# Performance work log

Measured on AMD Instinct MI355X. Metric: run time of the kernel, lower is better.

The kernel has to match this reference:

```python
import jax, jax.numpy as jnp
import numpy as np

D = 128  # head dim

def setup_inputs() -> dict:
    key = jax.random.key(0)
    k1, k2, k3, k4, k5 = jax.random.split(key, 5)
    B, N, M, C1, C2 = 4, 4096, 4096, 1024, 1024
    x = jax.random.normal(k1, (B, N, C1), dtype=jnp.float32)
    y = jax.random.normal(k2, (B, M, C2), dtype=jnp.float32)
    # Linear(c, d, bias=False): out = inp @ W where W is [c, d]
    Wq = jax.random.normal(k3, (C1, D), dtype=jnp.float32) / np.sqrt(C1)
    Wk = jax.random.normal(k4, (C2, D), dtype=jnp.float32) / np.sqrt(C2)
    Wv = jax.random.normal(k5, (C2, D), dtype=jnp.float32) / np.sqrt(C2)
    return {"x": x, "y": y, "Wq": Wq, "Wk": Wk, "Wv": Wv}

def reference(x, y, Wq, Wk, Wv):
    q = x @ Wq                               # [B, N, d]
    k = y @ Wk                               # [B, M, d]
    v = y @ Wv                               # [B, M, d]
    scale = 1.0 / jnp.sqrt(jnp.asarray(D, dtype=q.dtype))
    a = jnp.einsum('bnd,bmd->bnm', q, k) * scale
    a = jax.nn.softmax(a, axis=-1)           # softmax FIRST
    a = jnp.triu(a, k=1)                     # post-softmax causal mask (keeps strict upper)
    out = jnp.einsum('bnm,bmd->bnd', a, v)   # [B, N, d]
    return out
```

## Files before the change

### kernel.cpp

```cpp
#include <hip/hip_runtime.h>
#include <hip/hip_bf16.h>
#include <stdint.h>


typedef __attribute__((ext_vector_type(8))) __bf16    bf16x8;
typedef __attribute__((ext_vector_type(4))) float     floatx4;
typedef __attribute__((ext_vector_type(8))) uint16_t  u16x8;
typedef __attribute__((ext_vector_type(4))) uint32_t  u32x4;

#define DEVFN __device__ __forceinline__

DEVFN uint16_t f32_to_bf16(float f) {
  uint32_t u = __builtin_bit_cast(uint32_t, f);
  u += 0x7FFFu + ((u >> 16) & 1u);
  return (uint16_t)(u >> 16);
}

DEVFN uint32_t bcast(float f) { return __builtin_bit_cast(uint32_t, f); }

DEVFN uint32_t pack2_bf16(float a, float b) {
  return ((bcast(a) + 0x8000u) >> 16) | ((bcast(b) + 0x8000u) & 0xFFFF0000u);
}

DEVFN u32x4 pack_bf16_8(float4 a0, float4 a1) {
  u32x4 o;
  o[0] = pack2_bf16(a0.x, a0.y);
  o[1] = pack2_bf16(a0.z, a0.w);
  o[2] = pack2_bf16(a1.x, a1.y);
  o[3] = pack2_bf16(a1.z, a1.w);
  return o;
}

DEVFN void gl2lds16(const void* g, void* l) {
  __builtin_amdgcn_global_load_lds(
      (const __attribute__((address_space(1))) void*)g,
      (__attribute__((address_space(3))) void*)l, 16, 0, 0);
}

__global__ __launch_bounds__(256) void wt_kernel(
    const float* __restrict__ Wq, const float* __restrict__ Wk,
    const float* __restrict__ Wv, uint16_t* __restrict__ wt) {
  int tid = blockIdx.x * 256 + threadIdx.x;
  int mat = tid >> 14;
  int rem = tid & 16383;
  int n  = rem & 127;
  int k0 = rem >> 7;
  const float* W = (mat == 0) ? Wq : ((mat == 1) ? Wk : Wv);
  u16x8 v;
#pragma unroll
  for (int j = 0; j < 8; ++j) v[j] = f32_to_bf16(W[(k0 * 8 + j) * 128 + n]);
  *(u16x8*)&wt[mat * (128 * 1024) + n * 1024 + k0 * 8] = v;
}

__global__ __launch_bounds__(256) void qkv_kernel(
    const float* __restrict__ x, const float* __restrict__ y,
    const uint16_t* __restrict__ wt, uint16_t* __restrict__ q,
    uint16_t* __restrict__ k, uint16_t* __restrict__ vt) {
  constexpr int LDT = 72;
  constexpr int ABUF = 128 * LDT;
  __shared__ __align__(16) uint16_t sA[2 * ABUF];
  __shared__ __align__(16) uint16_t sW[2 * ABUF];
  const int t = threadIdx.x;
  const int mat = blockIdx.y, rt = blockIdx.x;
  const float* A = (mat == 0) ? x : y;
  const uint16_t* Wt = wt + mat * (128 * 1024);
  const int lane = t & 63, wv = t >> 6;
  const int cidx = lane & 15, quad = lane >> 4;
  const int sr = t >> 3;
  const int sc = (t & 7) * 8;
  const int Arow0 = rt * 128;

  floatx4 acc[2][8];
#pragma unroll
  for (int rg = 0; rg < 2; ++rg)
#pragma unroll
    for (int ng = 0; ng < 8; ++ng) acc[rg][ng] = (floatx4){0.f, 0.f, 0.f, 0.f};

  float4 a0r[4], a1r[4];
  u16x8 wr[4];
#pragma unroll
  for (int u = 0; u < 4; ++u) {
    int row = u * 32 + sr;
    const float* ap = &A[(size_t)(Arow0 + row) * 1024 + sc];
    a0r[u] = *(const float4*)ap;
    a1r[u] = *(const float4*)(ap + 4);
    wr[u]  = *(const u16x8*)&Wt[row * 1024 + sc];
  }
#pragma unroll
  for (int u = 0; u < 4; ++u) {
    int row = u * 32 + sr;
    *(u32x4*)&sA[row * LDT + sc] = pack_bf16_8(a0r[u], a1r[u]);
    *(u16x8*)&sW[row * LDT + sc] = wr[u];
  }
  __syncthreads();

  for (int kt = 0; kt < 16; ++kt) {
    const int cur = kt & 1, nxt = cur ^ 1;
    if (kt < 15) {
      const int kc = (kt + 1) * 64;
#pragma unroll
      for (int u = 0; u < 4; ++u) {
        int row = u * 32 + sr;
        const float* ap = &A[(size_t)(Arow0 + row) * 1024 + kc + sc];
        a0r[u] = *(const float4*)ap;
        a1r[u] = *(const float4*)(ap + 4);
        wr[u]  = *(const u16x8*)&Wt[row * 1024 + kc + sc];
      }
    }
    bf16x8 af[2][2];
#pragma unroll
    for (int rg = 0; rg < 2; ++rg)
#pragma unroll
      for (int ks = 0; ks < 2; ++ks)
        af[rg][ks] = *(const bf16x8*)
            &sA[cur * ABUF + (wv * 32 + rg * 16 + cidx) * LDT + ks * 32 + quad * 8];
#pragma unroll
    for (int ng = 0; ng < 8; ++ng) {
      bf16x8 b0 = *(const bf16x8*)&sW[cur * ABUF + (ng * 16 + cidx) * LDT + quad * 8];
      bf16x8 b1 = *(const bf16x8*)&sW[cur * ABUF + (ng * 16 + cidx) * LDT + 32 + quad * 8];
#pragma unroll
      for (int rg = 0; rg < 2; ++rg) {
        acc[rg][ng] = __builtin_amdgcn_mfma_f32_16x16x32_bf16(af[rg][0], b0, acc[rg][ng], 0, 0, 0);
        acc[rg][ng] = __builtin_amdgcn_mfma_f32_16x16x32_bf16(af[rg][1], b1, acc[rg][ng], 0, 0, 0);
      }
    }
    if (kt < 15) {
#pragma unroll
      for (int u = 0; u < 4; ++u) {
        int row = u * 32 + sr;
        *(u32x4*)&sA[nxt * ABUF + row * LDT + sc] = pack_bf16_8(a0r[u], a1r[u]);
        *(u16x8*)&sW[nxt * ABUF + row * LDT + sc] = wr[u];
      }
    }
    __syncthreads();
  }

  if (mat < 2) {
    uint16_t* outp = (mat == 0) ? q : k;
#pragma unroll
    for (int rg = 0; rg < 2; ++rg)
#pragma unroll
      for (int r = 0; r < 4; ++r) {
        int row = Arow0 + wv * 32 + rg * 16 + quad * 4 + r;
#pragma unroll
        for (int ng = 0; ng < 8; ++ng)
          outp[row * 128 + ng * 16 + cidx] = f32_to_bf16(acc[rg][ng][r]);
      }
  } else {
    int bq = rt >> 5;
    int mbase = (rt & 31) * 128;
#pragma unroll
    for (int rg = 0; rg < 2; ++rg)
#pragma unroll
      for (int r = 0; r < 4; ++r) {
        int m = mbase + wv * 32 + rg * 16 + quad * 4 + r;
#pragma unroll
        for (int ng = 0; ng < 8; ++ng)
          vt[(size_t)(bq * 128 + ng * 16 + cidx) * 4096 + m] = f32_to_bf16(acc[rg][ng][r]);
      }
  }
}

__global__ __launch_bounds__(256, 2) void attn_kernel(
    const uint16_t* __restrict__ q, const uint16_t* __restrict__ k,
    const uint16_t* __restrict__ vt, float* __restrict__ opart,
    float* __restrict__ lpart, int mlen, int iters) {
  constexpr int KB = 16384, VB = 16384;
  __shared__ __align__(16) uint8_t sK[2 * KB];
  __shared__ __align__(16) uint8_t sV[2 * VB];
  const int t = threadIdx.x;
  const int lane = t & 63, wv = t >> 6;
  const int cidx = lane & 15, quad = lane >> 4;
  const int qt = blockIdx.x, h = blockIdx.y, b = blockIdx.z;
  const int qmin = qt * 64 + wv * 16;
  const int mbase = h * mlen;

  const uint16_t* qb = q + (size_t)(b * 4096) * 128;
  const uint8_t* kb = (const uint8_t*)(k + (size_t)(b * 4096) * 128);
  const uint8_t* vb = (const uint8_t*)(vt + (size_t)(b * 128) * 4096);

  const float SC = 0.12751744610657223f;

  int kOffL[4], vOffL[4], kLds[4], vLds[4];
#pragma unroll
  for (int u = 0; u < 4; ++u) {
    int r  = wv * 16 + u * 4 + (lane >> 4);
    int g  = (lane & 15) ^ (r & 15);
    kOffL[u] = r * 256 + g * 16;
    kLds[u]  = (wv * 16 + u * 4) * 256;
    int rv = wv * 32 + u * 8 + (lane >> 3);
    int gv = (lane & 7) ^ (rv & 7);
    vOffL[u] = rv * 8192 + gv * 16;
    vLds[u]  = (wv * 32 + u * 8) * 128;
  }

  bf16x8 qf[4];
#pragma unroll
  for (int ks = 0; ks < 4; ++ks)
    qf[ks] = *(const bf16x8*)&qb[(qmin + cidx) * 128 + ks * 32 + quad * 8];

  floatx4 O[8];
#pragma unroll
  for (int dg = 0; dg < 8; ++dg) O[dg] = (floatx4){0.f, 0.f, 0.f, 0.f};
  float lsum = 0.f;

#pragma unroll
  for (int u = 0; u < 4; ++u) {
    gl2lds16(kb + (size_t)mbase * 256 + kOffL[u], sK + kLds[u]);
    gl2lds16(vb + (size_t)mbase * 2 + vOffL[u], sV + vLds[u]);
  }
  __syncthreads();

  for (int it = 0; it < iters; ++it) {
    const int m0 = mbase + it * 64;
    const int cur = it & 1, nxt = cur ^ 1;
    if (it + 1 < iters) {
      const int m1 = m0 + 64;
#pragma unroll
      for (int u = 0; u < 4; ++u) {
        gl2lds16(kb + (size_t)m1 * 256 + kOffL[u], sK + nxt * KB + kLds[u]);
        gl2lds16(vb + (size_t)m1 * 2 + vOffL[u], sV + nxt * VB + vLds[u]);
      }
    }

    floatx4 accST[4];
#pragma unroll
    for (int ng = 0; ng < 4; ++ng) accST[ng] = (floatx4){0.f, 0.f, 0.f, 0.f};
#pragma unroll
    for (int ks = 0; ks < 4; ++ks) {
      bf16x8 qv = qf[ks];
#pragma unroll
      for (int ng = 0; ng < 4; ++ng) {
        bf16x8 kf = *(const bf16x8*)
            (sK + cur * KB + (ng * 16 + cidx) * 256 + ((ks * 4 + quad) ^ cidx) * 16);
        accST[ng] = __builtin_amdgcn_mfma_f32_16x16x32_bf16(kf, qv, accST[ng], 0, 0, 0);
      }
    }

    float p[4][4];
#pragma unroll
    for (int ng = 0; ng < 4; ++ng)
#pragma unroll
      for (int r = 0; r < 4; ++r) {
        p[ng][r] = exp2f(accST[ng][r] * SC);
        lsum += p[ng][r];
      }

    if (m0 + 63 > qmin) {
      if (m0 < qmin + 16) {
#pragma unroll
        for (int ng = 0; ng < 4; ++ng)
#pragma unroll
          for (int r = 0; r < 4; ++r) {
            int m = m0 + ng * 16 + quad * 4 + r;
            int n = qmin + cidx;
            if (m <= n) p[ng][r] = 0.f;
          }
      }
      uint32_t pk[4][2];
#pragma unroll
      for (int ng = 0; ng < 4; ++ng) {
        pk[ng][0] = pack2_bf16(p[ng][0], p[ng][1]);
        pk[ng][1] = pack2_bf16(p[ng][2], p[ng][3]);
      }
#pragma unroll
      for (int ks = 0; ks < 2; ++ks) {
        u32x4 pbw;
#pragma unroll
        for (int j2 = 0; j2 < 4; ++j2) {
          int lr = ((quad & 1) << 3) + 2 * j2;
          int srcl = ((lr >> 2) << 4) + cidx;
          uint32_t lo = (uint32_t)__shfl((int)pk[2 * ks][j2 & 1], srcl);
          uint32_t hi = (uint32_t)__shfl((int)pk[2 * ks + 1][j2 & 1], srcl);
          pbw[j2] = (quad & 2) ? hi : lo;
        }
        bf16x8 pbv = __builtin_bit_cast(bf16x8, pbw);
#pragma unroll
        for (int dg = 0; dg < 8; ++dg) {
          bf16x8 vf = *(const bf16x8*)
              (sV + cur * VB + (dg * 16 + cidx) * 128 +
               (((ks * 4 + quad) ^ cidx) & 7) * 16);
          O[dg] = __builtin_amdgcn_mfma_f32_16x16x32_bf16(vf, pbv, O[dg], 0, 0, 0);
        }
      }
    }
    __syncthreads();
  }

  lsum += __shfl_xor(lsum, 16);
  lsum += __shfl_xor(lsum, 32);

  const int n = qmin + cidx;
  float* op = opart + ((size_t)h * 16384 + b * 4096 + n) * 128;
#pragma unroll
  for (int dg = 0; dg < 8; ++dg)
    *(float4*)&op[dg * 16 + quad * 4] = __builtin_bit_cast(float4, O[dg]);
  if (quad == 0) lpart[h * 16384 + b * 4096 + n] = lsum;
}

__global__ __launch_bounds__(256) void combine_kernel(
    const float* __restrict__ opart, const float* __restrict__ lpart,
    float* __restrict__ out, int hcount) {
  size_t i = (size_t)blockIdx.x * 256 + threadIdx.x;
  size_t e = i * 4;
  int row = (int)(e >> 7);
  float4 acc = {0.f, 0.f, 0.f, 0.f};
  float l = 0.f;
  for (int h = 0; h < hcount; ++h) {
    float4 ov = *(const float4*)&opart[(size_t)h * 2097152 + e];
    acc.x += ov.x; acc.y += ov.y; acc.z += ov.z; acc.w += ov.w;
    l += lpart[h * 16384 + row];
  }
  float inv = 1.0f / l;
  float4 o;
  o.x = acc.x * inv; o.y = acc.y * inv; o.z = acc.z * inv; o.w = acc.w * inv;
  *(float4*)&out[e] = o;
}

extern "C" void kernel_launch(void* const* d_in, const int* in_sizes, int n_in,
                              void* d_out, int out_size, void* d_ws, size_t ws_size,
                              hipStream_t stream) {
  const float* x  = (const float*)d_in[0];
  const float* y  = (const float*)d_in[1];
  const float* Wq = (const float*)d_in[2];
  const float* Wk = (const float*)d_in[3];
  const float* Wv = (const float*)d_in[4];
  uint16_t* ws = (uint16_t*)d_ws;
  uint16_t* wt = ws;
  uint16_t* q  = ws + 393216;
  uint16_t* k  = q + 2097152;
  uint16_t* vt = k + 2097152;
  float* opart = (float*)((char*)d_ws + 13369344);
  int hcount = (ws_size >= (size_t)13369344 + 4 * 8454144) ? 4 : 2;
  float* lpart = opart + (size_t)hcount * 2097152;
  float* o = (float*)d_out;
  int mlen = 4096 / hcount, iters = mlen / 64;

  hipLaunchKernelGGL(wt_kernel,      dim3(192),            dim3(256), 0, stream, Wq, Wk, Wv, wt);
  hipLaunchKernelGGL(qkv_kernel,     dim3(128, 3),         dim3(256), 0, stream, x, y, wt, q, k, vt);
  hipLaunchKernelGGL(attn_kernel,    dim3(64, hcount, 4),  dim3(256), 0, stream, q, k, vt, opart, lpart, mlen, iters);
  hipLaunchKernelGGL(combine_kernel, dim3(2048),           dim3(256), 0, stream, opart, lpart, o, hcount);
}
```

Measured before the change: 245.3 us.

## Process two 16-row query groups per wave to reuse K/V LDS fragments

Each wave now handles 32 query rows (two 16-row groups) instead of 16, so each block covers 128 queries and the grid's x dimension is halved. Every K and V fragment read from LDS feeds two MFMAs, halving LDS traffic and global K/V loads per query. The cost is roughly double the accumulator and Q register usage, which with launch bounds of 2 blocks/CU could cause spills, and there are half as many blocks, which lowers parallelism.

```diff
diff --git a/kernel.cpp b/kernel.cpp
--- a/kernel.cpp
+++ b/kernel.cpp
@@ -172,7 +172,7 @@
   const int lane = t & 63, wv = t >> 6;
   const int cidx = lane & 15, quad = lane >> 4;
   const int qt = blockIdx.x, h = blockIdx.y, b = blockIdx.z;
-  const int qmin = qt * 64 + wv * 16;
+  const int qmin = qt * 128 + wv * 32;
   const int mbase = h * mlen;
 
   const uint16_t* qb = q + (size_t)(b * 4096) * 128;
@@ -194,15 +194,20 @@
     vLds[u]  = (wv * 32 + u * 8) * 128;
   }
 
-  bf16x8 qf[4];
-#pragma unroll
-  for (int ks = 0; ks < 4; ++ks)
-    qf[ks] = *(const bf16x8*)&qb[(qmin + cidx) * 128 + ks * 32 + quad * 8];
-
-  floatx4 O[8];
-#pragma unroll
-  for (int dg = 0; dg < 8; ++dg) O[dg] = (floatx4){0.f, 0.f, 0.f, 0.f};
-  float lsum = 0.f;
+  bf16x8 qf[2][4];
+#pragma unroll
+  for (int qg = 0; qg < 2; ++qg)
+#pragma unroll
+    for (int ks = 0; ks < 4; ++ks)
+      qf[qg][ks] = *(const bf16x8*)
+          &qb[(qmin + qg * 16 + cidx) * 128 + ks * 32 + quad * 8];
+
+  floatx4 O[2][8];
+#pragma unroll
+  for (int qg = 0; qg < 2; ++qg)
+#pragma unroll
+    for (int dg = 0; dg < 8; ++dg) O[qg][dg] = (floatx4){0.f, 0.f, 0.f, 0.f};
+  float lsum[2] = {0.f, 0.f};
 
 #pragma unroll
   for (int u = 0; u < 4; ++u) {
@@ -223,79 +228,95 @@
       }
     }
 
-    floatx4 accST[4];
-#pragma unroll
-    for (int ng = 0; ng < 4; ++ng) accST[ng] = (floatx4){0.f, 0.f, 0.f, 0.f};
-#pragma unroll
-    for (int ks = 0; ks < 4; ++ks) {
-      bf16x8 qv = qf[ks];
+    floatx4 accST[2][4];
+#pragma unroll
+    for (int qg = 0; qg < 2; ++qg)
+#pragma unroll
+      for (int ng = 0; ng < 4; ++ng) accST[qg][ng] = (floatx4){0.f, 0.f, 0.f, 0.f};
+#pragma unroll
+    for (int ks = 0; ks < 4; ++ks)
 #pragma unroll
       for (int ng = 0; ng < 4; ++ng) {
         bf16x8 kf = *(const bf16x8*)
             (sK + cur * KB + (ng * 16 + cidx) * 256 + ((ks * 4 + quad) ^ cidx) * 16);
-        accST[ng] = __builtin_amdgcn_mfma_f32_16x16x32_bf16(kf, qv, accST[ng], 0, 0, 0);
-      }
-    }
-
-    float p[4][4];
-#pragma unroll
-    for (int ng = 0; ng < 4; ++ng)
-#pragma unroll
-      for (int r = 0; r < 4; ++r) {
-        p[ng][r] = exp2f(accST[ng][r] * SC);
-        lsum += p[ng][r];
-      }
+        accST[0][ng] = __builtin_amdgcn_mfma_f32_16x16x32_bf16(kf, qf[0][ks], accST[0][ng], 0, 0, 0);
+        accST[1][ng] = __builtin_amdgcn_mfma_f32_16x16x32_bf16(kf, qf[1][ks], accST[1][ng], 0, 0, 0);
+      }
+
+    float p[2][4][4];
+#pragma unroll
+    for (int qg = 0; qg < 2; ++qg)
+#pragma unroll
+      for (int ng = 0; ng < 4; ++ng)
+#pragma unroll
+        for (int r = 0; r < 4; ++r) {
+          p[qg][ng][r] = exp2f(accST[qg][ng][r] * SC);
+          lsum[qg] += p[qg][ng][r];
+        }
 
     if (m0 + 63 > qmin) {
-      if (m0 < qmin + 16) {
-#pragma unroll
-        for (int ng = 0; ng < 4; ++ng)
-#pragma unroll
-          for (int r = 0; r < 4; ++r) {
-            int m = m0 + ng * 16 + quad * 4 + r;
-            int n = qmin + cidx;
-            if (m <= n) p[ng][r] = 0.f;
+#pragma unroll
+      for (int qg = 0; qg < 2; ++qg) {
+        const int base = qmin + qg * 16;
+        if (m0 < base + 16) {
+#pragma unroll
+          for (int ng = 0; ng < 4; ++ng)
+#pragma unroll
+            for (int r = 0; r < 4; ++r) {
+              int m = m0 + ng * 16 + quad * 4 + r;
+              int n = base + cidx;
+              if (m <= n) p[qg][ng][r] = 0.f;
+            }
+        }
+      }
+      uint32_t pk[2][4][2];
+#pragma unroll
+      for (int qg = 0; qg < 2; ++qg)
+#pragma unroll
+        for (int ng = 0; ng < 4; ++ng) {
+          pk[qg][ng][0] = pack2_bf16(p[qg][ng][0], p[qg][ng][1]);
+          pk[qg][ng][1] = pack2_bf16(p[qg][ng][2], p[qg][ng][3]);
+        }
+#pragma unroll
+      for (int ks = 0; ks < 2; ++ks) {
+        bf16x8 pbv[2];
+#pragma unroll
+        for (int qg = 0; qg < 2; ++qg) {
+          u32x4 pbw;
+#pragma unroll
+          for (int j2 = 0; j2 < 4; ++j2) {
+            int lr = ((quad & 1) << 3) + 2 * j2;
+            int srcl = ((lr >> 2) << 4) + cidx;
+            uint32_t lo = (uint32_t)__shfl((int)pk[qg][2 * ks][j2 & 1], srcl);
+            uint32_t hi = (uint32_t)__shfl((int)pk[qg][2 * ks + 1][j2 & 1], srcl);
+            pbw[j2] = (quad & 2) ? hi : lo;
           }
-      }
-      uint32_t pk[4][2];
-#pragma unroll
-      for (int ng = 0; ng < 4; ++ng) {
-        pk[ng][0] = pack2_bf16(p[ng][0], p[ng][1]);
-        pk[ng][1] = pack2_bf16(p[ng][2], p[ng][3]);
-      }
-#pragma unroll
-      for (int ks = 0; ks < 2; ++ks) {
-        u32x4 pbw;
-#pragma unroll
-        for (int j2 = 0; j2 < 4; ++j2) {
-          int lr = ((quad & 1) << 3) + 2 * j2;
-          int srcl = ((lr >> 2) << 4) + cidx;
-          uint32_t lo = (uint32_t)__shfl((int)pk[2 * ks][j2 & 1], srcl);
-          uint32_t hi = (uint32_t)__shfl((int)pk[2 * ks + 1][j2 & 1], srcl);
-          pbw[j2] = (quad & 2) ? hi : lo;
-        }
-        bf16x8 pbv = __builtin_bit_cast(bf16x8, pbw);
+          pbv[qg] = __builtin_bit_cast(bf16x8, pbw);
+        }
 #pragma unroll
         for (int dg = 0; dg < 8; ++dg) {
           bf16x8 vf = *(const bf16x8*)
               (sV + cur * VB + (dg * 16 + cidx) * 128 +
                (((ks * 4 + quad) ^ cidx) & 7) * 16);
-          O[dg] = __builtin_amdgcn_mfma_f32_16x16x32_bf16(vf, pbv, O[dg], 0, 0, 0);
+          O[0][dg] = __builtin_amdgcn_mfma_f32_16x16x32_bf16(vf, pbv[0], O[0][dg], 0, 0, 0);
+          O[1][dg] = __builtin_amdgcn_mfma_f32_16x16x32_bf16(vf, pbv[1], O[1][dg], 0, 0, 0);
         }
       }
     }
     __syncthreads();
   }
 
-  lsum += __shfl_xor(lsum, 16);
-  lsum += __shfl_xor(lsum, 32);
-
-  const int n = qmin + cidx;
-  float* op = opart + ((size_t)h * 16384 + b * 4096 + n) * 128;
-#pragma unroll
-  for (int dg = 0; dg < 8; ++dg)
-    *(float4*)&op[dg * 16 + quad * 4] = __builtin_bit_cast(float4, O[dg]);
-  if (quad == 0) lpart[h * 16384 + b * 4096 + n] = lsum;
+#pragma unroll
+  for (int qg = 0; qg < 2; ++qg) {
+    lsum[qg] += __shfl_xor(lsum[qg], 16);
+    lsum[qg] += __shfl_xor(lsum[qg], 32);
+    const int n = qmin + qg * 16 + cidx;
+    float* op = opart + ((size_t)h * 16384 + b * 4096 + n) * 128;
+#pragma unroll
+    for (int dg = 0; dg < 8; ++dg)
+      *(float4*)&op[dg * 16 + quad * 4] = __builtin_bit_cast(float4, O[qg][dg]);
+    if (quad == 0) lpart[h * 16384 + b * 4096 + n] = lsum[qg];
+  }
 }
 
 __global__ __launch_bounds__(256) void combine_kernel(
@@ -338,6 +359,6 @@
 
   hipLaunchKernelGGL(wt_kernel,      dim3(192),            dim3(256), 0, stream, Wq, Wk, Wv, wt);
   hipLaunchKernelGGL(qkv_kernel,     dim3(128, 3),         dim3(256), 0, stream, x, y, wt, q, k, vt);
-  hipLaunchKernelGGL(attn_kernel,    dim3(64, hcount, 4),  dim3(256), 0, stream, q, k, vt, opart, lpart, mlen, iters);
+  hipLaunchKernelGGL(attn_kernel,    dim3(32, hcount, 4),  dim3(256), 0, stream, q, k, vt, opart, lpart, mlen, iters);
   hipLaunchKernelGGL(combine_kernel, dim3(2048),           dim3(256), 0, stream, opart, lpart, o, hcount);
 }
```

Result: faster. 233.7 us (-4.7%).
